# Optimization experiments

Measured on AMD Instinct MI355X. Metric: run time of the kernel, lower is better.

Reference implementation:

```python
import jax, jax.numpy as jnp
import numpy as np

BIG = 1e10  # sentinel for masked-out (padded) points, like pytorch3d's masking


def setup_inputs() -> dict:
    key = jax.random.key(0)
    k1, k2, k3, k4 = jax.random.split(key, 4)
    B, N, M = 16, 4096, 4096
    source_cloud = jax.random.normal(k1, (B, N, 2), dtype=jnp.float32)
    target_cloud = jax.random.normal(k2, (B, M, 2), dtype=jnp.float32)
    source_mask = jax.random.randint(k3, (B,), 0, N)  # lengths1
    target_mask = jax.random.randint(k4, (B,), 0, M)  # lengths2
    return {
        "source_cloud": source_cloud,
        "target_cloud": target_cloud,
        "source_mask": source_mask,
        "target_mask": target_mask,
    }


def reference(source_cloud, target_cloud, source_mask, target_mask):
    # source_cloud: [B, N, 2], target_cloud: [B, M, 2]
    # source_mask/target_mask: int lengths [B] (knn_points lengths1/lengths2)
    B, N, _ = source_cloud.shape
    M = target_cloud.shape[1]

    s2 = jnp.sum(source_cloud * source_cloud, axis=-1)  # [B, N]
    t2 = jnp.sum(target_cloud * target_cloud, axis=-1)  # [B, M]
    # squared pairwise distances [B, N, M]
    d2 = (s2[:, :, None] + t2[:, None, :]
          - 2.0 * jnp.einsum('bnd,bmd->bnm', source_cloud, target_cloud))

    src_valid = jnp.arange(N)[None, :] < source_mask[:, None]  # [B, N]
    tgt_valid = jnp.arange(M)[None, :] < target_mask[:, None]  # [B, M]

    # forward: for each source point, 1-NN over valid target points
    d2_fwd = jnp.where(tgt_valid[:, None, :], d2, BIG)
    min_fwd = jnp.maximum(jnp.min(d2_fwd, axis=-1), 0.0)  # [B, N]
    # backward: for each target point, 1-NN over valid source points
    d2_bwd = jnp.where(src_valid[:, :, None], d2, BIG)
    min_bwd = jnp.maximum(jnp.min(d2_bwd, axis=-2), 0.0)  # [B, M]

    # padded query points get dist 0 (pytorch3d knn_points semantics), then sqrt
    chamfer_forward = jnp.where(src_valid, jnp.sqrt(min_fwd), 0.0)
    chamfer_backward = jnp.where(tgt_valid, jnp.sqrt(min_bwd), 0.0)
    return (chamfer_forward, chamfer_backward)
```

## Files before the change

### kernel.cpp

```cpp
#include <hip/hip_runtime.h>


#define CHP 512
#define NQ  4
typedef float f2 __attribute__((ext_vector_type(2)));

__global__ __launch_bounds__(512, 2) void chamfer_fused(
    const float* __restrict__ src, const float* __restrict__ tgt,
    const int* __restrict__ slen, const int* __restrict__ tlen,
    float* __restrict__ out)
{
    __shared__ float4 sh_xy[CHP];
    __shared__ f2     sh_n[CHP];
    __shared__ float  sh_best[8][256];

    const int g    = blockIdx.x;
    const int tid  = threadIdx.x;
    const int row  = g & 31;
    const int qc   = g >> 5;
    const int dir  = row >> 4, b = row & 15;
    const int lane = tid & 63, w = tid >> 6;

    const int Lq = dir ? tlen[b] : slen[b];
    const int Lp = dir ? slen[b] : tlen[b];

    float* op = out + row * 4096 + qc * 256;

    if (qc * 256 >= Lq) {
        if (tid < 256) op[tid] = 0.f;
        return;
    }

    const float* Qp = dir ? tgt : src;
    const float* P  = dir ? src : tgt;

    float mx[NQ], my[NQ], s2q[NQ], best[NQ];
    #pragma unroll
    for (int k = 0; k < NQ; ++k) {
        const int q = qc * 256 + lane + k * 64;
        const float2 qv = ((const float2*)Qp)[b * 4096 + q];
        mx[k] = -2.f * qv.x;
        my[k] = -2.f * qv.y;
        s2q[k] = fmaf(qv.x, qv.x, qv.y * qv.y);
        best[k] = 1e10f;
    }

    const int npair = (Lp + 1) >> 1;
    const float4* Pp = (const float4*)P + b * 2048;

    for (int c0 = 0; c0 < npair; c0 += CHP) {
        const int npc = min(CHP, npair - c0);
        __syncthreads();
        if (tid < npc) {
            const float4 pp = Pp[c0 + tid];
            const int i0 = (c0 + tid) * 2;
            const float n0 = (i0 + 0 < Lp) ? fmaf(pp.x, pp.x, pp.y * pp.y) : 1e30f;
            const float n1 = (i0 + 1 < Lp) ? fmaf(pp.z, pp.z, pp.w * pp.w) : 1e30f;
            sh_xy[tid] = make_float4(pp.x, pp.z, pp.y, pp.w);
            sh_n[tid]  = f2{n0, n1};
        }
        __syncthreads();

        const int j0 = w * 64;
        const int j1 = min(j0 + 64, npc);
        #pragma unroll 8
        for (int j = j0; j < j1; ++j) {
            const float4 xy = sh_xy[j];
            const f2 np = sh_n[j];
            const f2 xp = f2{xy.x, xy.y};
            const f2 yp = f2{xy.z, xy.w};
            #pragma unroll
            for (int k = 0; k < NQ; ++k) {
                f2 v = xp * mx[k] + np;
                v = yp * my[k] + v;
                best[k] = fminf(best[k], fminf(v.x, v.y));
            }
        }
    }

    #pragma unroll
    for (int k = 0; k < NQ; ++k)
        sh_best[w][lane + k * 64] = best[k] + s2q[k];
    __syncthreads();

    if (tid < 256) {
        float m = sh_best[0][tid];
        #pragma unroll
        for (int ww = 1; ww < 8; ++ww)
            m = fminf(m, sh_best[ww][tid]);
        const int q = qc * 256 + tid;
        op[tid] = (q < Lq) ? sqrtf(fmaxf(m, 0.f)) : 0.f;
    }
}

extern "C" void kernel_launch(void* const* d_in, const int* in_sizes, int n_in,
                              void* d_out, int out_size, void* d_ws, size_t ws_size,
                              hipStream_t stream) {
    const float* src = (const float*)d_in[0];
    const float* tgt = (const float*)d_in[1];
    const int* slen  = (const int*)d_in[2];
    const int* tlen  = (const int*)d_in[3];
    (void)d_ws; (void)ws_size;

    chamfer_fused<<<512, 512, 0, stream>>>(src, tgt, slen, tlen, (float*)d_out);
}
```

Baseline: 90.29 us.

## Retile chamfer kernel: 8 queries per thread, 16-way point split, smaller blocks

Each thread now holds 8 query points instead of 4, and 16 groups of 16 threads each scan a 32-pair slice of the shared point chunk. Blocks shrink to 256 threads and the grid doubles to 1024 blocks with 128 queries per block. The aim is more register reuse of each shared-memory point load and finer work granularity across blocks, so ragged lengths balance better. The cost is a larger 16-way cross-group min reduction and higher register use. The change also handles an empty point set explicitly and changes grid-to-row mapping so consecutive blocks share a batch row.

```diff
diff --git a/kernel.cpp b/kernel.cpp
--- a/kernel.cpp
+++ b/kernel.cpp
@@ -2,47 +2,46 @@
 
 
 #define CHP 512
-#define NQ  4
+#define NQ  8
 typedef float f2 __attribute__((ext_vector_type(2)));
 
-__global__ __launch_bounds__(512, 2) void chamfer_fused(
+__global__ __launch_bounds__(256) void chamfer_one(
     const float* __restrict__ src, const float* __restrict__ tgt,
     const int* __restrict__ slen, const int* __restrict__ tlen,
     float* __restrict__ out)
 {
     __shared__ float4 sh_xy[CHP];
     __shared__ f2     sh_n[CHP];
-    __shared__ float  sh_best[8][256];
+    __shared__ float  sh_best[16][129];
 
     const int g    = blockIdx.x;
+    const int row  = g >> 5, slice = g & 31;
+    const int dir  = row >> 4, b = row & 15;
     const int tid  = threadIdx.x;
-    const int row  = g & 31;
-    const int qc   = g >> 5;
-    const int dir  = row >> 4, b = row & 15;
-    const int lane = tid & 63, w = tid >> 6;
 
     const int Lq = dir ? tlen[b] : slen[b];
     const int Lp = dir ? slen[b] : tlen[b];
 
-    float* op = out + row * 4096 + qc * 256;
+    float* op = out + row * 4096 + slice * 128;
 
-    if (qc * 256 >= Lq) {
-        if (tid < 256) op[tid] = 0.f;
+    if (slice * 128 >= Lq) {
+        if (tid < 128) op[tid] = 0.f;
         return;
     }
 
     const float* Qp = dir ? tgt : src;
     const float* P  = dir ? src : tgt;
 
+    const int qg = tid & 15, sh16 = tid >> 4;
+
     float mx[NQ], my[NQ], s2q[NQ], best[NQ];
     #pragma unroll
     for (int k = 0; k < NQ; ++k) {
-        const int q = qc * 256 + lane + k * 64;
-        const float2 qv = ((const float2*)Qp)[b * 4096 + q];
+        const float2 qv = ((const float2*)Qp)[b * 4096 + slice * 128 + qg * 8 + k];
         mx[k] = -2.f * qv.x;
         my[k] = -2.f * qv.y;
         s2q[k] = fmaf(qv.x, qv.x, qv.y * qv.y);
-        best[k] = 1e10f;
+        best[k] = 3.0e38f;
     }
 
     const int npair = (Lp + 1) >> 1;
@@ -51,19 +50,23 @@
     for (int c0 = 0; c0 < npair; c0 += CHP) {
         const int npc = min(CHP, npair - c0);
         __syncthreads();
-        if (tid < npc) {
-            const float4 pp = Pp[c0 + tid];
-            const int i0 = (c0 + tid) * 2;
-            const float n0 = (i0 + 0 < Lp) ? fmaf(pp.x, pp.x, pp.y * pp.y) : 1e30f;
-            const float n1 = (i0 + 1 < Lp) ? fmaf(pp.z, pp.z, pp.w * pp.w) : 1e30f;
-            sh_xy[tid] = make_float4(pp.x, pp.z, pp.y, pp.w);
-            sh_n[tid]  = f2{n0, n1};
+        #pragma unroll
+        for (int i = 0; i < 2; ++i) {
+            const int p = tid + i * 256;
+            if (p < npc) {
+                const float4 pp = Pp[c0 + p];
+                const int i0 = (c0 + p) * 2;
+                const float n0 = (i0 + 0 < Lp) ? fmaf(pp.x, pp.x, pp.y * pp.y) : 1e30f;
+                const float n1 = (i0 + 1 < Lp) ? fmaf(pp.z, pp.z, pp.w * pp.w) : 1e30f;
+                sh_xy[p] = make_float4(pp.x, pp.z, pp.y, pp.w);
+                sh_n[p]  = f2{n0, n1};
+            }
         }
         __syncthreads();
 
-        const int j0 = w * 64;
-        const int j1 = min(j0 + 64, npc);
-        #pragma unroll 8
+        const int j0 = sh16 * 32;
+        const int j1 = min(j0 + 32, npc);
+        #pragma unroll 4
         for (int j = j0; j < j1; ++j) {
             const float4 xy = sh_xy[j];
             const f2 np = sh_n[j];
@@ -80,16 +83,17 @@
 
     #pragma unroll
     for (int k = 0; k < NQ; ++k)
-        sh_best[w][lane + k * 64] = best[k] + s2q[k];
+        sh_best[sh16][qg * 8 + k] = best[k] + s2q[k];
     __syncthreads();
 
-    if (tid < 256) {
+    if (tid < 128) {
         float m = sh_best[0][tid];
         #pragma unroll
-        for (int ww = 1; ww < 8; ++ww)
-            m = fminf(m, sh_best[ww][tid]);
-        const int q = qc * 256 + tid;
-        op[tid] = (q < Lq) ? sqrtf(fmaxf(m, 0.f)) : 0.f;
+        for (int w = 1; w < 16; ++w)
+            m = fminf(m, sh_best[w][tid]);
+        const float d2 = (Lp == 0) ? 1e10f : m;
+        const int q = slice * 128 + tid;
+        op[tid] = (q < Lq) ? sqrtf(fmaxf(d2, 0.f)) : 0.f;
     }
 }
 
@@ -102,5 +106,5 @@
     const int* tlen  = (const int*)d_in[3];
     (void)d_ws; (void)ws_size;
 
-    chamfer_fused<<<512, 512, 0, stream>>>(src, tgt, slen, tlen, (float*)d_out);
+    chamfer_one<<<1024, 256, 0, stream>>>(src, tgt, slen, tlen, (float*)d_out);
 }
```

Result: no change. 89.00 us (-1.4%).
